# Optimization experiments

Hardware: AMD Instinct MI355X
Metric: run time of the kernel (lower is better)

Reference implementation:

```python
import jax, jax.numpy as jnp
import numpy as np

BN_EPS = 1e-5


def setup_inputs() -> dict:
    key = jax.random.key(0)
    ks = jax.random.split(key, 8)
    B, C, H, W = 8, 256, 64, 64
    Ci = 128
    s_in = 1.0 / np.sqrt(C)
    s_int = 1.0 / np.sqrt(Ci)
    return {
        "x": jax.random.normal(ks[0], (B, C, H, W), jnp.float32),
        "w_g": jax.random.normal(ks[1], (Ci, C), jnp.float32) * s_in,
        "b_g": jnp.zeros((Ci,), jnp.float32),
        "w_theta": jax.random.normal(ks[2], (Ci, C), jnp.float32) * s_in,
        "b_theta": jnp.zeros((Ci,), jnp.float32),
        "w_phi": jax.random.normal(ks[3], (Ci, C), jnp.float32) * s_in,
        "b_phi": jnp.zeros((Ci,), jnp.float32),
        "w_out": jax.random.normal(ks[4], (C, Ci), jnp.float32) * s_int,
        "b_out": jnp.zeros((C,), jnp.float32),
        "bn_gamma": jnp.ones((C,), jnp.float32),
        "bn_beta": jnp.zeros((C,), jnp.float32),
        "bn_mean": jnp.zeros((C,), jnp.float32),
        "bn_var": jnp.ones((C,), jnp.float32),
    }


def reference(x, w_g, b_g, w_theta, b_theta, w_phi, b_phi, w_out, b_out,
              bn_gamma, bn_beta, bn_mean, bn_var):
    B, C, H, W = x.shape
    Ci = w_g.shape[0]
    N = H * W
    # 1x1 convs == per-pixel linear projections
    g = (jnp.einsum('bchw,oc->bhwo', x, w_g) + b_g).reshape(B, N, Ci)
    theta = (jnp.einsum('bchw,oc->bhwo', x, w_theta) + b_theta).reshape(B, N, Ci)
    phi = (jnp.einsum('bchw,oc->bohw', x, w_phi) + b_phi[:, None, None]).reshape(B, Ci, N)
    # full N x N attention (no scaling, as in the original)
    att = jax.nn.softmax(jnp.einsum('bnc,bcm->bnm', theta, phi), axis=-1)
    y = jnp.einsum('bnm,bmc->bnc', att, g).reshape(B, H, W, Ci)
    # output 1x1 conv + inference-mode BatchNorm (per-channel affine)
    out = jnp.einsum('bhwc,oc->bohw', y, w_out) + b_out[:, None, None]
    inv = bn_gamma / jnp.sqrt(bn_var + BN_EPS)
    out = out * inv[:, None, None] + (bn_beta - bn_mean * inv)[:, None, None]
    return x + out
```

## Files before the change

### kernel.cpp

```cpp
#include <hip/hip_runtime.h>
#include <math.h>

#define BB 8
#define CC 256
#define CI 128
#define NN 4096
#define BN_EPS 1e-5f
#define LOG2E 1.4426950408889634f
#define FIXMAX 88.0f

typedef unsigned int uint;
typedef unsigned short ushort;
typedef __bf16 bf16x8 __attribute__((ext_vector_type(8)));
typedef _Float16 f16x8 __attribute__((ext_vector_type(8)));
typedef float f32x16 __attribute__((ext_vector_type(16)));

__device__ __forceinline__ ushort bfbits(float f) {
    return __builtin_bit_cast(ushort, (__bf16)f);
}
__device__ __forceinline__ ushort hbits(float f) {
    return __builtin_bit_cast(ushort, (_Float16)f);
}
__device__ __forceinline__ float bf2f(ushort h) {
    return __uint_as_float(((uint)h) << 16);
}
__device__ __forceinline__ float bflo(uint v) { return __uint_as_float(v << 16); }
__device__ __forceinline__ float bfhi(uint v) { return __uint_as_float(v & 0xffff0000u); }
__device__ __forceinline__ uint pk2(float a, float b) {
    return (uint)bfbits(a) | ((uint)bfbits(b) << 16);
}
__device__ __forceinline__ void gload16(const void* g, void* l) {
    __builtin_amdgcn_global_load_lds(
        (const __attribute__((address_space(1))) uint*)g,
        (__attribute__((address_space(3))) uint*)l, 16, 0, 0);
}
__device__ __forceinline__ bf16x8 asbf8(uint4 v) { return __builtin_bit_cast(bf16x8, v); }
__device__ __forceinline__ float fexp2(float a) {
    float e;
    asm("v_exp_f32 %0, %1" : "=v"(e) : "v"(a));
    return e;
}

__global__ __launch_bounds__(256) void wconv_kernel(
    const float* __restrict__ w_t, const float* __restrict__ w_p,
    const float* __restrict__ w_g, const float* __restrict__ w_o,
    const float* __restrict__ bn_g, const float* __restrict__ bn_b,
    const float* __restrict__ bn_m, const float* __restrict__ bn_v,
    const float* __restrict__ b_out,
    uint4* __restrict__ wt_h, uint4* __restrict__ wt_l,
    uint4* __restrict__ wp_h, uint4* __restrict__ wp_l,
    uint4* __restrict__ wg_h, uint4* __restrict__ wg_l,
    uint4* __restrict__ wo_h, uint4* __restrict__ wo_l,
    float* __restrict__ scale, float* __restrict__ shift)
{
    const int t = threadIdx.x, blk = blockIdx.x;
    if (blk == 64) {
        float inv = bn_g[t] * rsqrtf(bn_v[t] + BN_EPS);
        scale[t] = inv;
        shift[t] = b_out[t] * inv + bn_b[t] - bn_m[t] * inv;
        return;
    }
    int u = blk * 256 + t;
    int mat = u >> 12, ul = u & 4095;
    const float* src;
    uint4 *dh, *dl;
    int o, oct, C, O;
    if (mat == 0)      { src = w_t; dh = wt_h; dl = wt_l; }
    else if (mat == 1) { src = w_p; dh = wp_h; dl = wp_l; }
    else if (mat == 2) { src = w_g; dh = wg_h; dl = wg_l; }
    else               { src = w_o; dh = wo_h; dl = wo_l; }
    if (mat < 3) { O = 128; C = 256; o = ul >> 5; oct = ul & 31; }
    else         { O = 256; C = 128; o = ul >> 4; oct = ul & 15; }
    const float* s = src + (size_t)o * C + oct * 8;
    float4 va = *(const float4*)s, vb = *(const float4*)(s + 4);
    float v[8] = {va.x, va.y, va.z, va.w, vb.x, vb.y, vb.z, vb.w};
    uint hw[4], lw[4];
#pragma unroll
    for (int j = 0; j < 4; j++) {
        float a = v[2 * j], c = v[2 * j + 1];
        ushort ha = bfbits(a), hc = bfbits(c);
        hw[j] = (uint)ha | ((uint)hc << 16);
        lw[j] = pk2(a - bf2f(ha), c - bf2f(hc));
    }
    int di = oct * O + o;
    dh[di] = make_uint4(hw[0], hw[1], hw[2], hw[3]);
    dl[di] = make_uint4(lw[0], lw[1], lw[2], lw[3]);
}

__global__ __launch_bounds__(256, 2) void proj3_mfma(
    const float* __restrict__ x,
    const uint4* __restrict__ wt_h, const uint4* __restrict__ wt_l,
    const uint4* __restrict__ wp_h, const uint4* __restrict__ wp_l,
    const uint4* __restrict__ wg_h, const uint4* __restrict__ wg_l,
    const float* __restrict__ b_t, const float* __restrict__ b_p,
    const float* __restrict__ b_g,
    ushort* __restrict__ th, ushort* __restrict__ phi, ushort* __restrict__ gT)
{
    __shared__ __align__(16) char xsm[65536];
    const int t  = threadIdx.x;
    const int w  = t >> 6, l = t & 63;
    const int lq = l & 31, h = l >> 5;
    const int b  = blockIdx.x >> 6;
    const int n0 = (blockIdx.x & 63) << 6;

    {
        const int nq = t & 15;
#pragma unroll
        for (int i = 0; i < 2; i++) {
            int oct = (t >> 4) + 16 * i;
            const float* xp = x + ((size_t)b * CC + oct * 8) * NN + n0 + nq * 4;
            float4 r[8];
#pragma unroll
            for (int j = 0; j < 8; j++) r[j] = *(const float4*)(xp + (size_t)j * NN);
#pragma unroll
            for (int k = 0; k < 4; k++) {
                int n = nq * 4 + k;
                float v[8];
#pragma unroll
                for (int j = 0; j < 8; j++) v[j] = ((const float*)&r[j])[k];
                uint hw[4], lw[4];
#pragma unroll
                for (int j = 0; j < 4; j++) {
                    ushort ha = bfbits(v[2 * j]), hc = bfbits(v[2 * j + 1]);
                    hw[j] = (uint)ha | ((uint)hc << 16);
                    lw[j] = pk2(v[2 * j] - bf2f(ha), v[2 * j + 1] - bf2f(hc));
                }
                int uu = oct ^ (n & 31);
                *(uint4*)(xsm + n * 512 + uu * 16) = make_uint4(hw[0], hw[1], hw[2], hw[3]);
                *(uint4*)(xsm + 32768 + n * 512 + uu * 16) = make_uint4(lw[0], lw[1], lw[2], lw[3]);
            }
        }
    }
    __syncthreads();

    const int wo16 = w * 32 + lq;
    f32x16 acc[3][2];
    {
        float bt = b_t[wo16], bp = b_p[wo16];
        acc[0][0] = (f32x16)bt; acc[0][1] = (f32x16)bt;
        acc[1][0] = (f32x16)bp; acc[1][1] = (f32x16)bp;
        acc[2][0] = (f32x16)0.0f; acc[2][1] = (f32x16)0.0f;
    }

#pragma unroll 2
    for (int cs = 0; cs < 16; cs++) {
        int wi = (cs * 2 + h) * 128 + wo16;
        bf16x8 fth = asbf8(wt_h[wi]), ftl = asbf8(wt_l[wi]);
        bf16x8 fph = asbf8(wp_h[wi]), fpl = asbf8(wp_l[wi]);
        bf16x8 fgh = asbf8(wg_h[wi]), fgl = asbf8(wg_l[wi]);
        int xoff = lq * 512 + 16 * ((cs * 2 + h) ^ lq);
        bf16x8 xh0 = asbf8(*(const uint4*)(xsm + xoff));
        bf16x8 xh1 = asbf8(*(const uint4*)(xsm + 16384 + xoff));
        bf16x8 xl0 = asbf8(*(const uint4*)(xsm + 32768 + xoff));
        bf16x8 xl1 = asbf8(*(const uint4*)(xsm + 49152 + xoff));

        acc[0][0] = __builtin_amdgcn_mfma_f32_32x32x16_bf16(xh0, fth, acc[0][0], 0, 0, 0);
        acc[0][0] = __builtin_amdgcn_mfma_f32_32x32x16_bf16(xl0, fth, acc[0][0], 0, 0, 0);
        acc[0][0] = __builtin_amdgcn_mfma_f32_32x32x16_bf16(xh0, ftl, acc[0][0], 0, 0, 0);
        acc[0][1] = __builtin_amdgcn_mfma_f32_32x32x16_bf16(xh1, fth, acc[0][1], 0, 0, 0);
        acc[0][1] = __builtin_amdgcn_mfma_f32_32x32x16_bf16(xl1, fth, acc[0][1], 0, 0, 0);
        acc[0][1] = __builtin_amdgcn_mfma_f32_32x32x16_bf16(xh1, ftl, acc[0][1], 0, 0, 0);

        acc[1][0] = __builtin_amdgcn_mfma_f32_32x32x16_bf16(xh0, fph, acc[1][0], 0, 0, 0);
        acc[1][0] = __builtin_amdgcn_mfma_f32_32x32x16_bf16(xl0, fph, acc[1][0], 0, 0, 0);
        acc[1][0] = __builtin_amdgcn_mfma_f32_32x32x16_bf16(xh0, fpl, acc[1][0], 0, 0, 0);
        acc[1][1] = __builtin_amdgcn_mfma_f32_32x32x16_bf16(xh1, fph, acc[1][1], 0, 0, 0);
        acc[1][1] = __builtin_amdgcn_mfma_f32_32x32x16_bf16(xl1, fph, acc[1][1], 0, 0, 0);
        acc[1][1] = __builtin_amdgcn_mfma_f32_32x32x16_bf16(xh1, fpl, acc[1][1], 0, 0, 0);

        acc[2][0] = __builtin_amdgcn_mfma_f32_32x32x16_bf16(fgh, xh0, acc[2][0], 0, 0, 0);
        acc[2][0] = __builtin_amdgcn_mfma_f32_32x32x16_bf16(fgh, xl0, acc[2][0], 0, 0, 0);
        acc[2][0] = __builtin_amdgcn_mfma_f32_32x32x16_bf16(fgl, xh0, acc[2][0], 0, 0, 0);
        acc[2][1] = __builtin_amdgcn_mfma_f32_32x32x16_bf16(fgh, xh1, acc[2][1], 0, 0, 0);
        acc[2][1] = __builtin_amdgcn_mfma_f32_32x32x16_bf16(fgh, xl1, acc[2][1], 0, 0, 0);
        acc[2][1] = __builtin_amdgcn_mfma_f32_32x32x16_bf16(fgl, xh1, acc[2][1], 0, 0, 0);
    }

#pragma unroll
    for (int ns = 0; ns < 2; ns++) {
        size_t nb = (size_t)b * NN + n0 + ns * 32;
#pragma unroll
        for (int r = 0; r < 16; r++) {
            int nr = (r & 3) + 8 * (r >> 2) + 4 * h;
            size_t idx = (nb + nr) * CI + wo16;
            th[idx]  = hbits(acc[0][ns][r] * LOG2E);
            phi[idx] = hbits(acc[1][ns][r]);
        }
#pragma unroll
        for (int r = 0; r < 16; r++) {
            int orow = w * 32 + (r & 3) + 8 * (r >> 2) + 4 * h;
            gT[((size_t)b * CI + orow) * NN + n0 + ns * 32 + lq] =
                bfbits(acc[2][ns][r] + b_g[orow]);
        }
    }
}

__global__ __launch_bounds__(256, 2) void attn_mfma(
    const ushort* __restrict__ th, const ushort* __restrict__ phi,
    const ushort* __restrict__ gT,
    ushort* __restrict__ yP, float* __restrict__ lP)
{
    __shared__ __align__(16) char sm[65536];
    const int t  = threadIdx.x;
    const int w  = t >> 6, l = t & 63;
    const int lq = l & 31, h = l >> 5;
    const int b  = blockIdx.x & 7;
    const int qt = (blockIdx.x >> 3) & 31;
    const int kt = blockIdx.x >> 8;
    const int q0 = qt * 128 + w * 32;

    f16x8 thf[8];
    {
        const char* thp = (const char*)(th + ((size_t)b * NN + q0 + lq) * CI);
#pragma unroll
        for (int cs = 0; cs < 8; cs++)
            thf[cs] = __builtin_bit_cast(f16x8, *(const uint4*)(thp + cs * 32 + h * 16));
    }

    const char* phig = (const char*)(phi + (size_t)b * NN * CI);
    const char* gTg  = (const char*)(gT + (size_t)b * NN * CI);

    f32x16 ya[4];
#pragma unroll
    for (int ct = 0; ct < 4; ct++) ya[ct] = (f32x16)0.0f;
    float l_run = 0.0f;

    auto stage = [&](int buf, int tile) {
        const char* ps = phig + (size_t)tile * 16384;
        const char* gs = gTg + (size_t)tile * 128;
        char* lb = sm + buf * 32768;
#pragma unroll
        for (int j = 0; j < 4; j++) {
            int c  = w * 4 + j;
            int r  = c * 4 + (l >> 4);
            int cp = ((l & 15) * 16) ^ ((r & 15) << 4);
            gload16(ps + (size_t)r * 256 + cp, lb + c * 1024);
            int r8 = c * 8 + (l >> 3);
            int cg = ((l & 7) * 16) ^ ((r8 & 7) << 4);
            gload16(gs + (size_t)r8 * (NN * 2) + cg, lb + 16384 + c * 1024);
        }
    };

    const int t0 = kt * 32;
    stage(0, t0 + 0);
    stage(1, t0 + 1);
    asm volatile("s_waitcnt vmcnt(8)" ::: "memory");
    __builtin_amdgcn_s_barrier();
    __builtin_amdgcn_sched_barrier(0);

    const int swp = (lq & 15) << 4;
    const int swg = (lq & 7) << 4;

    for (int it = 0; it < 32; it++) {
        const char* smb = sm + (it & 1) * 32768;

        f32x16 sa0 = (f32x16)0.0f, sa1 = (f32x16)0.0f;
        __builtin_amdgcn_s_setprio(1);
#pragma unroll
        for (int cs = 0; cs < 8; cs++) {
            f16x8 f0 = __builtin_bit_cast(f16x8,
                *(const uint4*)(smb + lq * 256 + ((cs * 32 + h * 16) ^ swp)));
            f16x8 f1 = __builtin_bit_cast(f16x8,
                *(const uint4*)(smb + (32 + lq) * 256 + ((cs * 32 + h * 16) ^ swp)));
            sa0 = __builtin_amdgcn_mfma_f32_32x32x16_f16(f0, thf[cs], sa0, 0, 0, 0);
            sa1 = __builtin_amdgcn_mfma_f32_32x32x16_f16(f1, thf[cs], sa1, 0, 0, 0);
        }
        __builtin_amdgcn_s_setprio(0);

        {
            float t0s = 0.f, t1s = 0.f, t2s = 0.f, t3s = 0.f;
#pragma unroll
            for (int r = 0; r < 16; r += 4) {
                sa0[r]     = fexp2(sa0[r] - FIXMAX);     t0s += sa0[r];
                sa0[r + 1] = fexp2(sa0[r + 1] - FIXMAX); t1s += sa0[r + 1];
                sa0[r + 2] = fexp2(sa0[r + 2] - FIXMAX); t2s += sa0[r + 2];
                sa0[r + 3] = fexp2(sa0[r + 3] - FIXMAX); t3s += sa0[r + 3];
            }
#pragma unroll
            for (int r = 0; r < 16; r += 4) {
                sa1[r]     = fexp2(sa1[r] - FIXMAX);     t0s += sa1[r];
                sa1[r + 1] = fexp2(sa1[r + 1] - FIXMAX); t1s += sa1[r + 1];
                sa1[r + 2] = fexp2(sa1[r + 2] - FIXMAX); t2s += sa1[r + 2];
                sa1[r + 3] = fexp2(sa1[r + 3] - FIXMAX); t3s += sa1[r + 3];
            }
            l_run += (t0s + t1s) + (t2s + t3s);
        }

        __builtin_amdgcn_s_setprio(1);
#pragma unroll
        for (int mt = 0; mt < 2; mt++) {
            const f32x16& pa = mt ? sa1 : sa0;
#pragma unroll
            for (int s = 0; s < 2; s++) {
                const int base = s * 8;
                uint a0 = pk2(pa[base + 0], pa[base + 1]);
                uint a1 = pk2(pa[base + 2], pa[base + 3]);
                uint b0 = pk2(pa[base + 4], pa[base + 5]);
                uint b1 = pk2(pa[base + 6], pa[base + 7]);
                asm volatile("v_permlane32_swap_b32 %0, %1" : "+v"(a0), "+v"(b0));
                asm volatile("v_permlane32_swap_b32 %0, %1" : "+v"(a1), "+v"(b1));
                bf16x8 pf = __builtin_bit_cast(bf16x8, make_uint4(a0, a1, b0, b1));
                const int ks = mt * 2 + s;
#pragma unroll
                for (int ct = 0; ct < 4; ct++) {
                    bf16x8 gf = __builtin_bit_cast(bf16x8,
                        *(const uint4*)(smb + 16384 + (ct * 32 + lq) * 128 +
                                        ((ks * 32 + h * 16) ^ swg)));
                    ya[ct] = __builtin_amdgcn_mfma_f32_32x32x16_bf16(gf, pf, ya[ct], 0, 0, 0);
                }
            }
        }
        __builtin_amdgcn_s_setprio(0);

        asm volatile("" ::: "memory");
        __builtin_amdgcn_s_barrier();
        if (it < 30) {
            stage(it & 1, t0 + it + 2);
            asm volatile("s_waitcnt vmcnt(8)" ::: "memory");
            __builtin_amdgcn_s_barrier();
            __builtin_amdgcn_sched_barrier(0);
        } else if (it == 30) {
            asm volatile("s_waitcnt vmcnt(0)" ::: "memory");
            __builtin_amdgcn_s_barrier();
            __builtin_amdgcn_sched_barrier(0);
        }
    }

    float ltot = l_run + __shfl_xor(l_run, 32);
    if (h == 0) lP[((size_t)kt * 8 + b) * NN + q0 + lq] = ltot;
    float inv = 1.0f / ltot;

    ushort* yp = yP + (size_t)kt * ((size_t)BB * NN * CI);
    const size_t qb = ((size_t)b * NN + q0 + lq) * CI;
#pragma unroll
    for (int ct = 0; ct < 4; ct++)
#pragma unroll
        for (int r4 = 0; r4 < 4; r4++) {
            uint2 hw = make_uint2(
                pk2(ya[ct][r4 * 4 + 0] * inv, ya[ct][r4 * 4 + 1] * inv),
                pk2(ya[ct][r4 * 4 + 2] * inv, ya[ct][r4 * 4 + 3] * inv));
            int co = 32 * ct + 8 * r4 + 4 * h;
            *(uint2*)(yp + qb + co) = hw;
        }
}

__global__ __launch_bounds__(256) void ymerge_kernel(
    const ushort* __restrict__ yP, const float* __restrict__ lP,
    ushort* __restrict__ yh, ushort* __restrict__ yl)
{
    const size_t ARRL = (size_t)BB * NN;
    size_t g = (size_t)blockIdx.x * 256 + threadIdx.x;
    size_t row = g >> 4;
    int u = (int)(g & 15);

    float lA = lP[row], lB = lP[ARRL + row];
    float s = 1.0f / (lA + lB);
    float a = lA * s, c = lB * s;

    const uint4* y4 = (const uint4*)yP;
    uint4 va = y4[row * 16 + u];
    uint4 vb = y4[(ARRL * CI / 8) + row * 16 + u];
    const uint* pa = (const uint*)&va;
    const uint* pb = (const uint*)&vb;

    uint ho[4], lo[4];
#pragma unroll
    for (int j = 0; j < 4; j++) {
        float v0 = a * bflo(pa[j]) + c * bflo(pb[j]);
        float v1 = a * bfhi(pa[j]) + c * bfhi(pb[j]);
        ushort h0 = bfbits(v0), h1 = bfbits(v1);
        ho[j] = (uint)h0 | ((uint)h1 << 16);
        lo[j] = pk2(v0 - bf2f(h0), v1 - bf2f(h1));
    }
    ((uint4*)yh)[row * 16 + u] = make_uint4(ho[0], ho[1], ho[2], ho[3]);
    ((uint4*)yl)[row * 16 + u] = make_uint4(lo[0], lo[1], lo[2], lo[3]);
}

__global__ __launch_bounds__(256, 2) void outproj_mfma(
    const ushort* __restrict__ yh, const ushort* __restrict__ yl,
    const uint4* __restrict__ wo_h, const uint4* __restrict__ wo_l,
    const float* __restrict__ scale, const float* __restrict__ shift,
    const float* __restrict__ x, float* __restrict__ out)
{
    __shared__ __align__(16) char ysm[32768];
    const int t  = threadIdx.x;
    const int w  = t >> 6, l = t & 63;
    const int lq = l & 31, h = l >> 5;
    const int b  = blockIdx.x >> 6;
    const int n0 = (blockIdx.x & 63) << 6;

    {
#pragma unroll
        for (int j = 0; j < 4; j++) {
            int idx = w * 64 + j * 256 + l;
            int row = idx >> 4, u = idx & 15;
            size_t srow = ((size_t)b * NN + n0 + row) * CI;
            int cb = 16 * (u ^ (row & 15));
            gload16((const char*)yh + srow * 2 + cb, ysm + (w * 64 + j * 256) * 16);
            gload16((const char*)yl + srow * 2 + cb, ysm + 16384 + (w * 64 + j * 256) * 16);
        }
    }
    __syncthreads();

#pragma unroll
    for (int oi = 0; oi < 2; oi++) {
        const int ot = w + oi * 4;
        const int ob = ot * 32 + lq;
        f32x16 a0 = (f32x16)0.0f, a1 = (f32x16)0.0f;
#pragma unroll 2
        for (int cs = 0; cs < 8; cs++) {
            int wi = (cs * 2 + h) * 256 + ob;
            bf16x8 wfh = asbf8(wo_h[wi]), wfl = asbf8(wo_l[wi]);
            int xoff = lq * 256 + 16 * ((cs * 2 + h) ^ (lq & 15));
            bf16x8 y0h = asbf8(*(const uint4*)(ysm + xoff));
            bf16x8 y1h = asbf8(*(const uint4*)(ysm + 8192 + xoff));
            bf16x8 y0l = asbf8(*(const uint4*)(ysm + 16384 + xoff));
            bf16x8 y1l = asbf8(*(const uint4*)(ysm + 24576 + xoff));
            a0 = __builtin_amdgcn_mfma_f32_32x32x16_bf16(wfh, y0h, a0, 0, 0, 0);
            a0 = __builtin_amdgcn_mfma_f32_32x32x16_bf16(wfl, y0h, a0, 0, 0, 0);
            a0 = __builtin_amdgcn_mfma_f32_32x32x16_bf16(wfh, y0l, a0, 0, 0, 0);
            a1 = __builtin_amdgcn_mfma_f32_32x32x16_bf16(wfh, y1h, a1, 0, 0, 0);
            a1 = __builtin_amdgcn_mfma_f32_32x32x16_bf16(wfl, y1h, a1, 0, 0, 0);
            a1 = __builtin_amdgcn_mfma_f32_32x32x16_bf16(wfh, y1l, a1, 0, 0, 0);
        }
#pragma unroll
        for (int ns = 0; ns < 2; ns++) {
            const f32x16& av = ns ? a1 : a0;
#pragma unroll
            for (int r = 0; r < 16; r++) {
                int o = ot * 32 + (r & 3) + 8 * (r >> 2) + 4 * h;
                size_t ai = ((size_t)b * CC + o) * NN + n0 + ns * 32 + lq;
                out[ai] = av[r] * scale[o] + shift[o] + x[ai];
            }
        }
    }
}

extern "C" void kernel_launch(void* const* d_in, const int* in_sizes, int n_in,
                              void* d_out, int out_size, void* d_ws, size_t ws_size,
                              hipStream_t stream) {
    const float* x       = (const float*)d_in[0];
    const float* w_g     = (const float*)d_in[1];
    const float* b_g     = (const float*)d_in[2];
    const float* w_theta = (const float*)d_in[3];
    const float* b_theta = (const float*)d_in[4];
    const float* w_phi   = (const float*)d_in[5];
    const float* b_phi   = (const float*)d_in[6];
    const float* w_out   = (const float*)d_in[7];
    const float* b_out   = (const float*)d_in[8];
    const float* bn_g    = (const float*)d_in[9];
    const float* bn_b    = (const float*)d_in[10];
    const float* bn_m    = (const float*)d_in[11];
    const float* bn_v    = (const float*)d_in[12];
    float* out = (float*)d_out;

    const size_t arr = (size_t)BB * NN * CI;
    ushort* thw   = (ushort*)d_ws;
    ushort* phiw  = thw + arr;
    ushort* gTw   = phiw + arr;
    ushort* yPb   = gTw + arr;
    uint4*  wt_h  = (uint4*)(yPb + 2 * arr);
    uint4*  wt_l  = wt_h + 4096;
    uint4*  wp_h  = wt_l + 4096;
    uint4*  wp_l  = wp_h + 4096;
    uint4*  wg_h  = wp_l + 4096;
    uint4*  wg_l  = wg_h + 4096;
    uint4*  wo_h  = wg_l + 4096;
    uint4*  wo_l  = wo_h + 4096;
    float*  scl   = (float*)(wo_l + 4096);
    float*  shf   = scl + 256;
    float*  lPb   = shf + 256;
    ushort* yhb   = thw;
    ushort* ylb   = phiw;

    wconv_kernel<<<65, 256, 0, stream>>>(
        w_theta, w_phi, w_g, w_out, bn_g, bn_b, bn_m, bn_v, b_out,
        wt_h, wt_l, wp_h, wp_l, wg_h, wg_l, wo_h, wo_l, scl, shf);
    proj3_mfma<<<BB * 64, 256, 0, stream>>>(
        x, wt_h, wt_l, wp_h, wp_l, wg_h, wg_l, b_theta, b_phi, b_g,
        thw, phiw, gTw);
    attn_mfma<<<512, 256, 0, stream>>>(thw, phiw, gTw, yPb, lPb);
    ymerge_kernel<<<2048, 256, 0, stream>>>(yPb, lPb, yhb, ylb);
    outproj_mfma<<<BB * 64, 256, 0, stream>>>(
        yhb, ylb, wo_h, wo_l, scl, shf, x, out);
}
```

Before: 144.4 us.

## Fuse split-K merge into output projection and retile attention to 64-query blocks

Removes the separate ymerge kernel. The output projection now loads both split-K attention partials directly, runs MFMA on each one, and combines them with weights normalised from the two row sums in the epilogue. This saves a full read/write pass over the intermediate y and one kernel launch, at the cost of extra MFMAs and dropping the low-order residual of y. Separately, attention uses 128-thread blocks with 64 queries and 32-key tiles staged in half the LDS. That doubles the grid and lets more blocks fit per CU, but it also doubles the number of barrier-synchronised iterations.

```diff
diff --git a/kernel.cpp b/kernel.cpp
--- a/kernel.cpp
+++ b/kernel.cpp
@@ -24,8 +24,6 @@
 __device__ __forceinline__ float bf2f(ushort h) {
     return __uint_as_float(((uint)h) << 16);
 }
-__device__ __forceinline__ float bflo(uint v) { return __uint_as_float(v << 16); }
-__device__ __forceinline__ float bfhi(uint v) { return __uint_as_float(v & 0xffff0000u); }
 __device__ __forceinline__ uint pk2(float a, float b) {
     return (uint)bfbits(a) | ((uint)bfbits(b) << 16);
 }
@@ -195,19 +193,19 @@
     }
 }
 
-__global__ __launch_bounds__(256, 2) void attn_mfma(
+__global__ __launch_bounds__(128, 2) void attn_mfma(
     const ushort* __restrict__ th, const ushort* __restrict__ phi,
     const ushort* __restrict__ gT,
     ushort* __restrict__ yP, float* __restrict__ lP)
 {
-    __shared__ __align__(16) char sm[65536];
+    __shared__ __align__(16) char sm[32768];
     const int t  = threadIdx.x;
     const int w  = t >> 6, l = t & 63;
     const int lq = l & 31, h = l >> 5;
     const int b  = blockIdx.x & 7;
-    const int qt = (blockIdx.x >> 3) & 31;
-    const int kt = blockIdx.x >> 8;
-    const int q0 = qt * 128 + w * 32;
+    const int qt = (blockIdx.x >> 3) & 63;
+    const int kt = blockIdx.x >> 9;
+    const int q0 = qt * 64 + w * 32;
 
     f16x8 thf[8];
     {
@@ -226,22 +224,22 @@
     float l_run = 0.0f;
 
     auto stage = [&](int buf, int tile) {
-        const char* ps = phig + (size_t)tile * 16384;
-        const char* gs = gTg + (size_t)tile * 128;
-        char* lb = sm + buf * 32768;
+        const char* ps = phig + (size_t)tile * 8192;
+        const char* gs = gTg + (size_t)tile * 64;
+        char* lb = sm + buf * 16384;
 #pragma unroll
         for (int j = 0; j < 4; j++) {
             int c  = w * 4 + j;
             int r  = c * 4 + (l >> 4);
             int cp = ((l & 15) * 16) ^ ((r & 15) << 4);
             gload16(ps + (size_t)r * 256 + cp, lb + c * 1024);
-            int r8 = c * 8 + (l >> 3);
-            int cg = ((l & 7) * 16) ^ ((r8 & 7) << 4);
-            gload16(gs + (size_t)r8 * (NN * 2) + cg, lb + 16384 + c * 1024);
+            int r8 = c * 16 + (l >> 2);
+            int cg = ((l & 3) * 16) ^ ((r8 & 3) << 4);
+            gload16(gs + (size_t)r8 * (NN * 2) + cg, lb + 8192 + c * 1024);
         }
     };
 
-    const int t0 = kt * 32;
+    const int t0 = kt * 64;
     stage(0, t0 + 0);
     stage(1, t0 + 1);
     asm volatile("s_waitcnt vmcnt(8)" ::: "memory");
@@ -249,21 +247,18 @@
     __builtin_amdgcn_sched_barrier(0);
 
     const int swp = (lq & 15) << 4;
-    const int swg = (lq & 7) << 4;
-
-    for (int it = 0; it < 32; it++) {
-        const char* smb = sm + (it & 1) * 32768;
-
-        f32x16 sa0 = (f32x16)0.0f, sa1 = (f32x16)0.0f;
+    const int swg = (lq & 3) << 4;
+
+    for (int it = 0; it < 64; it++) {
+        const char* smb = sm + (it & 1) * 16384;
+
+        f32x16 sa0 = (f32x16)0.0f;
         __builtin_amdgcn_s_setprio(1);
 #pragma unroll
         for (int cs = 0; cs < 8; cs++) {
             f16x8 f0 = __builtin_bit_cast(f16x8,
                 *(const uint4*)(smb + lq * 256 + ((cs * 32 + h * 16) ^ swp)));
-            f16x8 f1 = __builtin_bit_cast(f16x8,
-                *(const uint4*)(smb + (32 + lq) * 256 + ((cs * 32 + h * 16) ^ swp)));
             sa0 = __builtin_amdgcn_mfma_f32_32x32x16_f16(f0, thf[cs], sa0, 0, 0, 0);
-            sa1 = __builtin_amdgcn_mfma_f32_32x32x16_f16(f1, thf[cs], sa1, 0, 0, 0);
         }
         __builtin_amdgcn_s_setprio(0);
 
@@ -276,50 +271,38 @@
                 sa0[r + 2] = fexp2(sa0[r + 2] - FIXMAX); t2s += sa0[r + 2];
                 sa0[r + 3] = fexp2(sa0[r + 3] - FIXMAX); t3s += sa0[r + 3];
             }
-#pragma unroll
-            for (int r = 0; r < 16; r += 4) {
-                sa1[r]     = fexp2(sa1[r] - FIXMAX);     t0s += sa1[r];
-                sa1[r + 1] = fexp2(sa1[r + 1] - FIXMAX); t1s += sa1[r + 1];
-                sa1[r + 2] = fexp2(sa1[r + 2] - FIXMAX); t2s += sa1[r + 2];
-                sa1[r + 3] = fexp2(sa1[r + 3] - FIXMAX); t3s += sa1[r + 3];
-            }
             l_run += (t0s + t1s) + (t2s + t3s);
         }
 
         __builtin_amdgcn_s_setprio(1);
 #pragma unroll
-        for (int mt = 0; mt < 2; mt++) {
-            const f32x16& pa = mt ? sa1 : sa0;
-#pragma unroll
-            for (int s = 0; s < 2; s++) {
-                const int base = s * 8;
-                uint a0 = pk2(pa[base + 0], pa[base + 1]);
-                uint a1 = pk2(pa[base + 2], pa[base + 3]);
-                uint b0 = pk2(pa[base + 4], pa[base + 5]);
-                uint b1 = pk2(pa[base + 6], pa[base + 7]);
-                asm volatile("v_permlane32_swap_b32 %0, %1" : "+v"(a0), "+v"(b0));
-                asm volatile("v_permlane32_swap_b32 %0, %1" : "+v"(a1), "+v"(b1));
-                bf16x8 pf = __builtin_bit_cast(bf16x8, make_uint4(a0, a1, b0, b1));
-                const int ks = mt * 2 + s;
-#pragma unroll
-                for (int ct = 0; ct < 4; ct++) {
-                    bf16x8 gf = __builtin_bit_cast(bf16x8,
-                        *(const uint4*)(smb + 16384 + (ct * 32 + lq) * 128 +
-                                        ((ks * 32 + h * 16) ^ swg)));
-                    ya[ct] = __builtin_amdgcn_mfma_f32_32x32x16_bf16(gf, pf, ya[ct], 0, 0, 0);
-                }
+        for (int s = 0; s < 2; s++) {
+            const int base = s * 8;
+            uint a0 = pk2(sa0[base + 0], sa0[base + 1]);
+            uint a1 = pk2(sa0[base + 2], sa0[base + 3]);
+            uint b0 = pk2(sa0[base + 4], sa0[base + 5]);
+            uint b1 = pk2(sa0[base + 6], sa0[base + 7]);
+            asm volatile("v_permlane32_swap_b32 %0, %1" : "+v"(a0), "+v"(b0));
+            asm volatile("v_permlane32_swap_b32 %0, %1" : "+v"(a1), "+v"(b1));
+            bf16x8 pf = __builtin_bit_cast(bf16x8, make_uint4(a0, a1, b0, b1));
+#pragma unroll
+            for (int ct = 0; ct < 4; ct++) {
+                bf16x8 gf = __builtin_bit_cast(bf16x8,
+                    *(const uint4*)(smb + 8192 + (ct * 32 + lq) * 64 +
+                                    ((s * 32 + h * 16) ^ swg)));
+                ya[ct] = __builtin_amdgcn_mfma_f32_32x32x16_bf16(gf, pf, ya[ct], 0, 0, 0);
             }
         }
         __builtin_amdgcn_s_setprio(0);
 
         asm volatile("" ::: "memory");
         __builtin_amdgcn_s_barrier();
-        if (it < 30) {
+        if (it < 62) {
             stage(it & 1, t0 + it + 2);
             asm volatile("s_waitcnt vmcnt(8)" ::: "memory");
             __builtin_amdgcn_s_barrier();
             __builtin_amdgcn_sched_barrier(0);
-        } else if (it == 30) {
+        } else if (it == 62) {
             asm volatile("s_waitcnt vmcnt(0)" ::: "memory");
             __builtin_amdgcn_s_barrier();
             __builtin_amdgcn_sched_barrier(0);
@@ -344,40 +327,8 @@
         }
 }
 
-__global__ __launch_bounds__(256) void ymerge_kernel(
+__global__ __launch_bounds__(256, 2) void outproj_mfma(
     const ushort* __restrict__ yP, const float* __restrict__ lP,
-    ushort* __restrict__ yh, ushort* __restrict__ yl)
-{
-    const size_t ARRL = (size_t)BB * NN;
-    size_t g = (size_t)blockIdx.x * 256 + threadIdx.x;
-    size_t row = g >> 4;
-    int u = (int)(g & 15);
-
-    float lA = lP[row], lB = lP[ARRL + row];
-    float s = 1.0f / (lA + lB);
-    float a = lA * s, c = lB * s;
-
-    const uint4* y4 = (const uint4*)yP;
-    uint4 va = y4[row * 16 + u];
-    uint4 vb = y4[(ARRL * CI / 8) + row * 16 + u];
-    const uint* pa = (const uint*)&va;
-    const uint* pb = (const uint*)&vb;
-
-    uint ho[4], lo[4];
-#pragma unroll
-    for (int j = 0; j < 4; j++) {
-        float v0 = a * bflo(pa[j]) + c * bflo(pb[j]);
-        float v1 = a * bfhi(pa[j]) + c * bfhi(pb[j]);
-        ushort h0 = bfbits(v0), h1 = bfbits(v1);
-        ho[j] = (uint)h0 | ((uint)h1 << 16);
-        lo[j] = pk2(v0 - bf2f(h0), v1 - bf2f(h1));
-    }
-    ((uint4*)yh)[row * 16 + u] = make_uint4(ho[0], ho[1], ho[2], ho[3]);
-    ((uint4*)yl)[row * 16 + u] = make_uint4(lo[0], lo[1], lo[2], lo[3]);
-}
-
-__global__ __launch_bounds__(256, 2) void outproj_mfma(
-    const ushort* __restrict__ yh, const ushort* __restrict__ yl,
     const uint4* __restrict__ wo_h, const uint4* __restrict__ wo_l,
     const float* __restrict__ scale, const float* __restrict__ shift,
     const float* __restrict__ x, float* __restrict__ out)
@@ -388,6 +339,7 @@
     const int lq = l & 31, h = l >> 5;
     const int b  = blockIdx.x >> 6;
     const int n0 = (blockIdx.x & 63) << 6;
+    const size_t arr = (size_t)BB * NN * CI;
 
     {
 #pragma unroll
@@ -396,41 +348,56 @@
             int row = idx >> 4, u = idx & 15;
             size_t srow = ((size_t)b * NN + n0 + row) * CI;
             int cb = 16 * (u ^ (row & 15));
-            gload16((const char*)yh + srow * 2 + cb, ysm + (w * 64 + j * 256) * 16);
-            gload16((const char*)yl + srow * 2 + cb, ysm + 16384 + (w * 64 + j * 256) * 16);
+            gload16((const char*)yP + srow * 2 + cb, ysm + (w * 64 + j * 256) * 16);
+            gload16((const char*)(yP + arr) + srow * 2 + cb,
+                    ysm + 16384 + (w * 64 + j * 256) * 16);
         }
     }
     __syncthreads();
+
+    float lA0 = lP[(size_t)b * NN + n0 + lq];
+    float lB0 = lP[(size_t)(8 + b) * NN + n0 + lq];
+    float lA1 = lP[(size_t)b * NN + n0 + 32 + lq];
+    float lB1 = lP[(size_t)(8 + b) * NN + n0 + 32 + lq];
+    float i0 = 1.0f / (lA0 + lB0), i1 = 1.0f / (lA1 + lB1);
+    float aA0 = lA0 * i0, aB0 = lB0 * i0;
+    float aA1 = lA1 * i1, aB1 = lB1 * i1;
 
 #pragma unroll
     for (int oi = 0; oi < 2; oi++) {
         const int ot = w + oi * 4;
         const int ob = ot * 32 + lq;
-        f32x16 a0 = (f32x16)0.0f, a1 = (f32x16)0.0f;
+        f32x16 cA0 = (f32x16)0.0f, cA1 = (f32x16)0.0f;
+        f32x16 cB0 = (f32x16)0.0f, cB1 = (f32x16)0.0f;
 #pragma unroll 2
         for (int cs = 0; cs < 8; cs++) {
             int wi = (cs * 2 + h) * 256 + ob;
             bf16x8 wfh = asbf8(wo_h[wi]), wfl = asbf8(wo_l[wi]);
             int xoff = lq * 256 + 16 * ((cs * 2 + h) ^ (lq & 15));
-            bf16x8 y0h = asbf8(*(const uint4*)(ysm + xoff));
-            bf16x8 y1h = asbf8(*(const uint4*)(ysm + 8192 + xoff));
-            bf16x8 y0l = asbf8(*(const uint4*)(ysm + 16384 + xoff));
-            bf16x8 y1l = asbf8(*(const uint4*)(ysm + 24576 + xoff));
-            a0 = __builtin_amdgcn_mfma_f32_32x32x16_bf16(wfh, y0h, a0, 0, 0, 0);
-            a0 = __builtin_amdgcn_mfma_f32_32x32x16_bf16(wfl, y0h, a0, 0, 0, 0);
-            a0 = __builtin_amdgcn_mfma_f32_32x32x16_bf16(wfh, y0l, a0, 0, 0, 0);
-            a1 = __builtin_amdgcn_mfma_f32_32x32x16_bf16(wfh, y1h, a1, 0, 0, 0);
-            a1 = __builtin_amdgcn_mfma_f32_32x32x16_bf16(wfl, y1h, a1, 0, 0, 0);
-            a1 = __builtin_amdgcn_mfma_f32_32x32x16_bf16(wfh, y1l, a1, 0, 0, 0);
+            bf16x8 yA0 = asbf8(*(const uint4*)(ysm + xoff));
+            bf16x8 yA1 = asbf8(*(const uint4*)(ysm + 8192 + xoff));
+            bf16x8 yB0 = asbf8(*(const uint4*)(ysm + 16384 + xoff));
+            bf16x8 yB1 = asbf8(*(const uint4*)(ysm + 24576 + xoff));
+            cA0 = __builtin_amdgcn_mfma_f32_32x32x16_bf16(wfh, yA0, cA0, 0, 0, 0);
+            cA0 = __builtin_amdgcn_mfma_f32_32x32x16_bf16(wfl, yA0, cA0, 0, 0, 0);
+            cB0 = __builtin_amdgcn_mfma_f32_32x32x16_bf16(wfh, yB0, cB0, 0, 0, 0);
+            cB0 = __builtin_amdgcn_mfma_f32_32x32x16_bf16(wfl, yB0, cB0, 0, 0, 0);
+            cA1 = __builtin_amdgcn_mfma_f32_32x32x16_bf16(wfh, yA1, cA1, 0, 0, 0);
+            cA1 = __builtin_amdgcn_mfma_f32_32x32x16_bf16(wfl, yA1, cA1, 0, 0, 0);
+            cB1 = __builtin_amdgcn_mfma_f32_32x32x16_bf16(wfh, yB1, cB1, 0, 0, 0);
+            cB1 = __builtin_amdgcn_mfma_f32_32x32x16_bf16(wfl, yB1, cB1, 0, 0, 0);
         }
 #pragma unroll
         for (int ns = 0; ns < 2; ns++) {
-            const f32x16& av = ns ? a1 : a0;
+            const f32x16& avA = ns ? cA1 : cA0;
+            const f32x16& avB = ns ? cB1 : cB0;
+            const float aA = ns ? aA1 : aA0;
+            const float aB = ns ? aB1 : aB0;
 #pragma unroll
             for (int r = 0; r < 16; r++) {
                 int o = ot * 32 + (r & 3) + 8 * (r >> 2) + 4 * h;
                 size_t ai = ((size_t)b * CC + o) * NN + n0 + ns * 32 + lq;
-                out[ai] = av[r] * scale[o] + shift[o] + x[ai];
+                out[ai] = (aA * avA[r] + aB * avB[r]) * scale[o] + shift[o] + x[ai];
             }
         }
     }
@@ -470,8 +437,6 @@
     float*  scl   = (float*)(wo_l + 4096);
     float*  shf   = scl + 256;
     float*  lPb   = shf + 256;
-    ushort* yhb   = thw;
-    ushort* ylb   = phiw;
 
     wconv_kernel<<<65, 256, 0, stream>>>(
         w_theta, w_phi, w_g, w_out, bn_g, bn_b, bn_m, bn_v, b_out,
@@ -479,8 +444,7 @@
     proj3_mfma<<<BB * 64, 256, 0, stream>>>(
         x, wt_h, wt_l, wp_h, wp_l, wg_h, wg_l, b_theta, b_phi, b_g,
         thw, phiw, gTw);
-    attn_mfma<<<512, 256, 0, stream>>>(thw, phiw, gTw, yPb, lPb);
-    ymerge_kernel<<<2048, 256, 0, stream>>>(yPb, lPb, yhb, ylb);
+    attn_mfma<<<1024, 128, 0, stream>>>(thw, phiw, gTw, yPb, lPb);
     outproj_mfma<<<BB * 64, 256, 0, stream>>>(
-        yhb, ylb, wo_h, wo_l, scl, shf, x, out);
-}
+        yPb, lPb, wo_h, wo_l, scl, shf, x, out);
+}
```

New measurement: 154.2 us. +6.8%, slower.
